# Kernel tuning notes

Measured on AMD Instinct MI355X. Metric: run time of the kernel, lower is better.

Reference implementation:

```python
import jax, jax.numpy as jnp
import numpy as np

BN_EPS = 1e-5
DIST_EPS = 1e-8


def setup_inputs() -> dict:
    key = jax.random.key(0)
    ks = jax.random.split(key, 8)
    B, N, M = 8, 8192, 2048
    C1, C2 = 128, 256
    Cin = C1 + C2  # 384
    H = 256
    return {
        "xyz1": jax.random.normal(ks[0], (B, N, 3), dtype=jnp.float32),
        "xyz2": jax.random.normal(ks[1], (B, M, 3), dtype=jnp.float32),
        "points1": jax.random.normal(ks[2], (B, N, C1), dtype=jnp.float32),
        "points2": jax.random.normal(ks[3], (B, M, C2), dtype=jnp.float32),
        "W1": jax.random.normal(ks[4], (H, Cin), dtype=jnp.float32) * 0.05,
        "b1": jnp.zeros((H,), dtype=jnp.float32),
        "gamma1": jnp.ones((H,), dtype=jnp.float32),
        "beta1": jnp.zeros((H,), dtype=jnp.float32),
        "W2": jax.random.normal(ks[5], (H, H), dtype=jnp.float32) * 0.05,
        "b2": jnp.zeros((H,), dtype=jnp.float32),
        "gamma2": jnp.ones((H,), dtype=jnp.float32),
        "beta2": jnp.zeros((H,), dtype=jnp.float32),
    }


def _interpolate(xyz1, xyz2, points2):
    # squared distances (B,N,M) via the bmm expansion, as in square_distance
    d = (jnp.sum(xyz1 * xyz1, -1)[:, :, None]
         + jnp.sum(xyz2 * xyz2, -1)[:, None, :]
         - 2.0 * jnp.einsum("bnc,bmc->bnm", xyz1, xyz2))
    neg, idx = jax.lax.top_k(-d, 3)          # 3 smallest distances
    dists = -neg                              # (B,N,3)
    recip = 1.0 / (dists + DIST_EPS)
    w = recip / jnp.sum(recip, -1, keepdims=True)  # (B,N,3)
    gathered = jax.vmap(lambda p, i: p[i])(points2, idx)  # (B,N,3,C2)
    return jnp.einsum("bnkc,bnk->bnc", gathered, w)


def _conv_bn_relu(x, W, b, gamma, beta):
    # pointwise conv1d: (B,N,Cin) x (Cout,Cin) -> (B,N,Cout)
    y = jnp.einsum("bnc,oc->bno", x, W) + b
    mean = jnp.mean(y, axis=(0, 1))           # BatchNorm1d (training-mode batch stats)
    var = jnp.var(y, axis=(0, 1))
    y = (y - mean) * jax.lax.rsqrt(var + BN_EPS) * gamma + beta
    return jax.nn.relu(y)


def reference(xyz1, xyz2, points1, points2, W1, b1, gamma1, beta1, W2, b2, gamma2, beta2):
    interp = _interpolate(xyz1, xyz2, points2)          # (B,N,C2)
    x = jnp.concatenate([points1, interp], axis=-1)     # (B,N,C1+C2)
    x = _conv_bn_relu(x, W1, b1, gamma1, beta1)
    x = _conv_bn_relu(x, W2, b2, gamma2, beta2)
    return x  # (B,N,mlp[-1])
```

## Files before the change

kernel.cpp:

```cpp
#include <hip/hip_runtime.h>
#include <hip/hip_bf16.h>
#include <stdint.h>

#define B_SZ  8
#define N_Q   8192
#define M_PT  2048
#define C1    128
#define C2    256
#define CIN   384
#define H_OUT 256
#define R_TOT 65536

#define NCH   8
#define CHM   (M_PT / NCH)
#define QPB   32

typedef __bf16 bf16x8 __attribute__((ext_vector_type(8)));
typedef __bf16 bf16x4 __attribute__((ext_vector_type(4)));
typedef __bf16 bf16x2 __attribute__((ext_vector_type(2)));
typedef float  f32x4  __attribute__((ext_vector_type(4)));

__device__ __forceinline__ void async_copy16(const void* g, void* l) {
    __builtin_amdgcn_global_load_lds(
        (const __attribute__((address_space(1))) unsigned int*)g,
        (__attribute__((address_space(3))) unsigned int*)l,
        16, 0, 0);
}

__global__ __launch_bounds__(256) void f2bf2(const float* __restrict__ a, int na,
                                             const float* __restrict__ b, int nb,
                                             __bf16* __restrict__ oa,
                                             __bf16* __restrict__ ob) {
    int i = blockIdx.x * 256 + threadIdx.x;
    if (i < na)            oa[i] = (__bf16)a[i];
    else if (i - na < nb)  ob[i - na] = (__bf16)b[i - na];
}

__global__ __launch_bounds__(256) void knn_vals(
    const float* __restrict__ xyz1, const float* __restrict__ xyz2,
    float4* __restrict__ vals4) {
    __shared__ float4 pos[CHM];
    const int tid = threadIdx.x;
    const int c   = blockIdx.x & (NCH - 1);
    const int qb  = (blockIdx.x >> 3) & 31;
    const int b   = blockIdx.x >> 8;
    {
        const float* x2 = xyz2 + ((size_t)b * M_PT + c * CHM) * 3;
        float x = x2[tid * 3], y = x2[tid * 3 + 1], z = x2[tid * 3 + 2];
        pos[tid] = make_float4(-2.f * x, -2.f * y, -2.f * z,
                               fmaf(x, x, fmaf(y, y, z * z)));
    }
    __syncthreads();

    const int q = b * N_Q + qb * 256 + tid;
    const float* q1 = xyz1 + (size_t)q * 3;
    float x1 = q1[0], y1 = q1[1], z1 = q1[2];
    float v0 = 3.4e38f, v1 = 3.4e38f, v2 = 3.4e38f;
#pragma unroll 8
    for (int j = 0; j < CHM; ++j) {
        float4 p = pos[j];
        float d  = fmaf(p.x, x1, fmaf(p.y, y1, fmaf(p.z, z1, p.w)));
        float n0 = fminf(d, v0);
        float n1 = __builtin_amdgcn_fmed3f(d, v0, v1);
        float n2 = __builtin_amdgcn_fmed3f(d, v1, v2);
        v0 = n0; v1 = n1; v2 = n2;
    }
    vals4[(size_t)c * R_TOT + q] = make_float4(v0, v1, v2, 0.f);
}

__global__ __launch_bounds__(256) void knn_merge(
    const float4* __restrict__ vals4, const float* __restrict__ xyz1,
    float4* __restrict__ v4, float4* __restrict__ w4) {
    const int q = blockIdx.x * 256 + threadIdx.x;
    float v0 = 3.4e38f, v1 = 3.4e38f, v2 = 3.4e38f;
#pragma unroll
    for (int c = 0; c < NCH; ++c) {
        float4 t = vals4[(size_t)c * R_TOT + q];
#pragma unroll
        for (int k = 0; k < 3; ++k) {
            float d  = (k == 0) ? t.x : (k == 1) ? t.y : t.z;
            float n0 = fminf(d, v0);
            float n1 = __builtin_amdgcn_fmed3f(d, v0, v1);
            float n2 = __builtin_amdgcn_fmed3f(d, v1, v2);
            v0 = n0; v1 = n1; v2 = n2;
        }
    }
    const float* q1 = xyz1 + (size_t)q * 3;
    float x1 = q1[0], y1 = q1[1], z1 = q1[2];
    float n1q = fmaf(x1, x1, fmaf(y1, y1, z1 * z1));
    float r0 = 1.f / ((v0 + n1q) + 1e-8f);
    float r1 = 1.f / ((v1 + n1q) + 1e-8f);
    float r2 = 1.f / ((v2 + n1q) + 1e-8f);
    float rs = 1.f / (r0 + r1 + r2);
    v4[q] = make_float4(v0, v1, v2, 0.f);
    w4[q] = make_float4(r0 * rs, r1 * rs, r2 * rs, 0.f);
}

__global__ __launch_bounds__(256) void knn_recover(
    const float* __restrict__ xyz1, const float* __restrict__ xyz2,
    const float4* __restrict__ v4, int4* __restrict__ ci4) {
    __shared__ float4 pos[CHM];
    const int tid = threadIdx.x;
    const int c   = blockIdx.x & (NCH - 1);
    const int qb  = (blockIdx.x >> 3) & 31;
    const int b   = blockIdx.x >> 8;
    {
        const float* x2 = xyz2 + ((size_t)b * M_PT + c * CHM) * 3;
        float x = x2[tid * 3], y = x2[tid * 3 + 1], z = x2[tid * 3 + 2];
        pos[tid] = make_float4(-2.f * x, -2.f * y, -2.f * z,
                               fmaf(x, x, fmaf(y, y, z * z)));
    }
    __syncthreads();

    const int q = b * N_Q + qb * 256 + tid;
    const float* q1 = xyz1 + (size_t)q * 3;
    float x1 = q1[0], y1 = q1[1], z1 = q1[2];
    const float4 vv = v4[q];
    int i0 = 0x7fffffff, i1 = 0x7fffffff, i2 = 0x7fffffff;
    const int jb = c * CHM;
#pragma unroll 4
    for (int j = 0; j < CHM; ++j) {
        float4 p = pos[j];
        float d  = fmaf(p.x, x1, fmaf(p.y, y1, fmaf(p.z, z1, p.w)));
        if (d <= vv.z) {
            const int jj = jb + j;
            i0 = min(i0, (d == vv.x) ? jj : 0x7fffffff);
            i1 = min(i1, (d == vv.y) ? jj : 0x7fffffff);
            i2 = min(i2, (d == vv.z) ? jj : 0x7fffffff);
        }
    }
    ci4[(size_t)c * R_TOT + q] = make_int4(i0, i1, i2, 0);
}

__global__ __launch_bounds__(256) void interp_gather(
    const float* __restrict__ p1,  const float* __restrict__ p2,
    const int4* __restrict__ ci4,  const float4* __restrict__ w4,
    __bf16* __restrict__ xb) {
    __shared__ float wgt[QPB * 3];
    __shared__ int   ids[QPB * 3];

    const int tid = threadIdx.x;
    const int b   = blockIdx.x >> 8;
    const int q0  = (blockIdx.x & 255) * QPB;

    if (tid < QPB) {
        const int q = b * N_Q + q0 + tid;
        int i0 = 0x7fffffff, i1 = 0x7fffffff, i2 = 0x7fffffff;
#pragma unroll
        for (int c = 0; c < NCH; ++c) {
            int4 t = ci4[(size_t)c * R_TOT + q];
            i0 = min(i0, t.x); i1 = min(i1, t.y); i2 = min(i2, t.z);
        }
        float4 w = w4[q];
        wgt[tid * 3] = w.x; wgt[tid * 3 + 1] = w.y; wgt[tid * 3 + 2] = w.z;
        ids[tid * 3] = i0;  ids[tid * 3 + 1] = i1;  ids[tid * 3 + 2] = i2;
    }
    __syncthreads();

    const int wave = tid >> 6, lane = tid & 63;
    const float* p2b = p2 + (size_t)b * M_PT * C2;
    const float* p1b = p1 + (size_t)(b * N_Q + q0) * C1;
    __bf16* outp = xb + (size_t)(b * N_Q + q0) * CIN;
    for (int qq = wave; qq < QPB; qq += 4) {
        float w0 = wgt[qq * 3], w1 = wgt[qq * 3 + 1], w2 = wgt[qq * 3 + 2];
        int   j0 = ids[qq * 3], j1 = ids[qq * 3 + 1], j2 = ids[qq * 3 + 2];
        const float4* ra = (const float4*)(p2b + (size_t)j0 * C2);
        const float4* rb = (const float4*)(p2b + (size_t)j1 * C2);
        const float4* rc = (const float4*)(p2b + (size_t)j2 * C2);
        float4 va = ra[lane], vb = rb[lane], vc = rc[lane];
        bf16x4 o;
        o[0] = (__bf16)(w0 * va.x + w1 * vb.x + w2 * vc.x);
        o[1] = (__bf16)(w0 * va.y + w1 * vb.y + w2 * vc.y);
        o[2] = (__bf16)(w0 * va.z + w1 * vb.z + w2 * vc.z);
        o[3] = (__bf16)(w0 * va.w + w1 * vb.w + w2 * vc.w);
        *(bf16x4*)(outp + (size_t)qq * CIN + C1 + lane * 4) = o;
        float2 pv = ((const float2*)(p1b + (size_t)qq * C1))[lane];
        bf16x2 o2; o2[0] = (__bf16)pv.x; o2[1] = (__bf16)pv.y;
        *(bf16x2*)(outp + (size_t)qq * CIN + lane * 2) = o2;
    }
}

template <int K, bool OUT_BF16>
__global__ __launch_bounds__(256, 2) void gemm_bt(const __bf16* __restrict__ A,
                                                  const __bf16* __restrict__ Bw,
                                                  void* __restrict__ Cout,
                                                  float* __restrict__ partS,
                                                  float* __restrict__ partQ) {
    __shared__ __attribute__((aligned(16))) __bf16 As[128 * 32];
    __shared__ __attribute__((aligned(16))) __bf16 Bs[128 * 32];
    const int tid  = threadIdx.x;
    const int wave = tid >> 6, lane = tid & 63;
    const int wm = wave >> 1, wn = wave & 1;
    const int quad = lane >> 4, r16 = lane & 15;
    const int bx = blockIdx.x & 1, by = blockIdx.x >> 1;
    const int l4 = lane >> 2, lk = (lane & 3) * 8;

    f32x4 acc[4][4] = {};

    const __bf16* gA = A  + (size_t)(by * 128 + wave * 32 + l4) * K + lk;
    const __bf16* gB = Bw + (size_t)(bx * 128 + wave * 32 + l4) * K + lk;
    char* lA = (char*)As + wave * 2048;
    char* lB = (char*)Bs + wave * 2048;

    for (int k0 = 0; k0 < K; k0 += 32) {
        async_copy16(gA + k0,                  lA);
        async_copy16(gA + k0 + (size_t)16 * K, lA + 1024);
        async_copy16(gB + k0,                  lB);
        async_copy16(gB + k0 + (size_t)16 * K, lB + 1024);
        __syncthreads();

        bf16x8 af[4], bf[4];
#pragma unroll
        for (int t = 0; t < 4; ++t)
            af[t] = *(const bf16x8*)(As + (wm * 64 + t * 16 + r16) * 32 + quad * 8);
#pragma unroll
        for (int u = 0; u < 4; ++u)
            bf[u] = *(const bf16x8*)(Bs + (wn * 64 + u * 16 + r16) * 32 + quad * 8);
#pragma unroll
        for (int t = 0; t < 4; ++t)
#pragma unroll
            for (int u = 0; u < 4; ++u)
                acc[t][u] = __builtin_amdgcn_mfma_f32_16x16x32_bf16(af[t], bf[u], acc[t][u], 0, 0, 0);
        __syncthreads();
    }

#pragma unroll
    for (int t = 0; t < 4; ++t) {
#pragma unroll
        for (int u = 0; u < 4; ++u) {
            const int col = bx * 128 + wn * 64 + u * 16 + r16;
#pragma unroll
            for (int r = 0; r < 4; ++r) {
                const int row = by * 128 + wm * 64 + t * 16 + quad * 4 + r;
                if (OUT_BF16)
                    ((__bf16*)Cout)[(size_t)row * H_OUT + col] = (__bf16)acc[t][u][r];
                else
                    ((float*)Cout)[(size_t)row * H_OUT + col] = acc[t][u][r];
            }
        }
    }

    float* redS = (float*)As;
    float* redQ = ((float*)As) + 1024;
    const int slot = wm * 4 + quad;
#pragma unroll
    for (int u = 0; u < 4; ++u) {
        float s = 0.f, qq = 0.f;
#pragma unroll
        for (int t = 0; t < 4; ++t)
#pragma unroll
            for (int r = 0; r < 4; ++r) { float v = acc[t][u][r]; s += v; qq = fmaf(v, v, qq); }
        const int col = wn * 64 + u * 16 + r16;
        redS[col * 8 + slot] = s;
        redQ[col * 8 + slot] = qq;
    }
    __syncthreads();
    if (tid < 128) {
        float s = 0.f, qq = 0.f;
#pragma unroll
        for (int k = 0; k < 8; ++k) { s += redS[tid * 8 + k]; qq += redQ[tid * 8 + k]; }
        partS[(size_t)blockIdx.x * 128 + tid] = s;
        partQ[(size_t)blockIdx.x * 128 + tid] = qq;
    }
}

__global__ __launch_bounds__(256) void bn_finalize(const float* __restrict__ pS,
                                                   const float* __restrict__ pQ,
                                                   const float* __restrict__ gamma,
                                                   const float* __restrict__ beta,
                                                   float* __restrict__ sc,
                                                   float* __restrict__ sh) {
    __shared__ float rs[256], rq[256];
    const int c = blockIdx.x;
    const int t = threadIdx.x;
    const int half = c >> 7, lo = c & 127;
    const size_t o1 = (size_t)(2 * t + half) * 128 + lo;
    const size_t o2 = (size_t)(2 * (t + 256) + half) * 128 + lo;
    rs[t] = pS[o1] + pS[o2];
    rq[t] = pQ[o1] + pQ[o2];
    __syncthreads();
    for (int k = 128; k > 0; k >>= 1) {
        if (t < k) { rs[t] += rs[t + k]; rq[t] += rq[t + k]; }
        __syncthreads();
    }
    if (t == 0) {
        const float inv = 1.f / (float)R_TOT;
        float mean = rs[0] * inv;
        float var  = rq[0] * inv - mean * mean;
        float a    = gamma[c] * rsqrtf(var + 1e-5f);
        sc[c] = a;
        sh[c] = beta[c] - mean * a;
    }
}

__global__ __launch_bounds__(256) void apply_bf16(__bf16* __restrict__ y,
                                                  const float* __restrict__ sc,
                                                  const float* __restrict__ sh) {
    __shared__ float scs[256], shs[256];
    scs[threadIdx.x] = sc[threadIdx.x];
    shs[threadIdx.x] = sh[threadIdx.x];
    __syncthreads();
    size_t i = ((size_t)blockIdx.x * 256 + threadIdx.x) * 8;
    int c0 = (int)(i & 255);
    bf16x8 v = *(const bf16x8*)(y + i);
#pragma unroll
    for (int e = 0; e < 8; ++e) {
        float f = fmaf((float)v[e], scs[c0 + e], shs[c0 + e]);
        v[e] = (__bf16)fmaxf(f, 0.f);
    }
    *(bf16x8*)(y + i) = v;
}

__global__ __launch_bounds__(256) void apply_f32(float* __restrict__ y,
                                                 const float* __restrict__ sc,
                                                 const float* __restrict__ sh) {
    __shared__ float scs[256], shs[256];
    scs[threadIdx.x] = sc[threadIdx.x];
    shs[threadIdx.x] = sh[threadIdx.x];
    __syncthreads();
    size_t i = ((size_t)blockIdx.x * 256 + threadIdx.x) * 4;
    int c0 = (int)(i & 255);
    float4 v = *(const float4*)(y + i);
    v.x = fmaxf(fmaf(v.x, scs[c0 + 0], shs[c0 + 0]), 0.f);
    v.y = fmaxf(fmaf(v.y, scs[c0 + 1], shs[c0 + 1]), 0.f);
    v.z = fmaxf(fmaf(v.z, scs[c0 + 2], shs[c0 + 2]), 0.f);
    v.w = fmaxf(fmaf(v.w, scs[c0 + 3], shs[c0 + 3]), 0.f);
    *(float4*)(y + i) = v;
}

extern "C" void kernel_launch(void* const* d_in, const int* in_sizes, int n_in,
                              void* d_out, int out_size, void* d_ws, size_t ws_size,
                              hipStream_t stream) {
    const float* xyz1 = (const float*)d_in[0];
    const float* xyz2 = (const float*)d_in[1];
    const float* p1   = (const float*)d_in[2];
    const float* p2   = (const float*)d_in[3];
    const float* W1   = (const float*)d_in[4];
    const float* g1   = (const float*)d_in[6];
    const float* be1  = (const float*)d_in[7];
    const float* W2   = (const float*)d_in[8];
    const float* g2   = (const float*)d_in[10];
    const float* be2  = (const float*)d_in[11];
    float* out = (float*)d_out;

    char* ws = (char*)d_ws;
    __bf16* xb     = (__bf16*)(ws);
    __bf16* y1b    = (__bf16*)(ws + 50331648);
    float4* vals4  = (float4*)(ws + 50331648);
    int4*   ci4    = (int4*)  (ws + 58720256);
    float4* v4     = (float4*)(ws + 67108864);
    float4* w4     = (float4*)(ws + 68157440);
    __bf16* wb1    = (__bf16*)(ws + 83886080);
    __bf16* wb2    = (__bf16*)(ws + 84082688);
    float*  sc1    = (float*) (ws + 84213760);
    float*  sh1    = sc1 + 256;
    float*  sc2    = sc1 + 512;
    float*  sh2    = sc1 + 768;

    float* partS1 = (float*)d_out;
    float* partQ1 = partS1 + 131072;
    float* partS2 = (float*)ws;
    float* partQ2 = partS2 + 131072;

    f2bf2<<<640, 256, 0, stream>>>(W1, H_OUT * CIN, W2, H_OUT * H_OUT, wb1, wb2);

    knn_vals<<<B_SZ * 32 * NCH, 256, 0, stream>>>(xyz1, xyz2, vals4);
    knn_merge<<<R_TOT / 256, 256, 0, stream>>>(vals4, xyz1, v4, w4);
    knn_recover<<<B_SZ * 32 * NCH, 256, 0, stream>>>(xyz1, xyz2, v4, ci4);
    interp_gather<<<R_TOT / QPB, 256, 0, stream>>>(p1, p2, ci4, w4, xb);

    gemm_bt<CIN, true><<<1024, 256, 0, stream>>>(xb, wb1, (void*)y1b, partS1, partQ1);
    bn_finalize<<<256, 256, 0, stream>>>(partS1, partQ1, g1, be1, sc1, sh1);
    apply_bf16<<<8192, 256, 0, stream>>>(y1b, sc1, sh1);

    gemm_bt<H_OUT, false><<<1024, 256, 0, stream>>>(y1b, wb2, (void*)out, partS2, partQ2);
    bn_finalize<<<256, 256, 0, stream>>>(partS2, partQ2, g2, be2, sc2, sh2);
    apply_f32<<<16384, 256, 0, stream>>>(out, sc2, sh2);
}
```

Baseline: 280.4 us.

## Fuse KNN stages into one kernel and store second GEMM output as bf16

The chunked KNN pipeline (vals, merge, recover) and the weight conversion kernel are merged into a single kernel in which each block scans all 2048 points from LDS. That block computes the weights and recovers the indices directly, so the partial-result buffers and the merge pass disappear. The second GEMM now writes bf16 to workspace, and the final BN/ReLU kernel reads bf16 and writes fp32 output, halving the intermediate traffic. The cost is that the KNN grid shrinks from 2048 to 256 blocks, which risks under-occupying the GPU on the compute-bound distance scan, and the extra bf16 rounding of the final pre-BN values may reduce accuracy.

```diff
diff --git a/kernel.cpp b/kernel.cpp
--- a/kernel.cpp
+++ b/kernel.cpp
@@ -11,8 +11,6 @@
 #define H_OUT 256
 #define R_TOT 65536
 
-#define NCH   8
-#define CHM   (M_PT / NCH)
 #define QPB   32
 
 typedef __bf16 bf16x8 __attribute__((ext_vector_type(8)));
@@ -27,37 +25,38 @@
         16, 0, 0);
 }
 
-__global__ __launch_bounds__(256) void f2bf2(const float* __restrict__ a, int na,
-                                             const float* __restrict__ b, int nb,
-                                             __bf16* __restrict__ oa,
-                                             __bf16* __restrict__ ob) {
-    int i = blockIdx.x * 256 + threadIdx.x;
-    if (i < na)            oa[i] = (__bf16)a[i];
-    else if (i - na < nb)  ob[i - na] = (__bf16)b[i - na];
-}
-
-__global__ __launch_bounds__(256) void knn_vals(
+__global__ __launch_bounds__(256) void knn_fused(
     const float* __restrict__ xyz1, const float* __restrict__ xyz2,
-    float4* __restrict__ vals4) {
-    __shared__ float4 pos[CHM];
+    const float* __restrict__ W1,   const float* __restrict__ W2,
+    __bf16* __restrict__ wb1,       __bf16* __restrict__ wb2,
+    float4* __restrict__ w4,        int4* __restrict__ ci4) {
+    __shared__ float4 pos[M_PT];
     const int tid = threadIdx.x;
-    const int c   = blockIdx.x & (NCH - 1);
-    const int qb  = (blockIdx.x >> 3) & 31;
-    const int b   = blockIdx.x >> 8;
+    const int b   = blockIdx.x >> 5;
+    const int qb  = blockIdx.x & 31;
+
     {
-        const float* x2 = xyz2 + ((size_t)b * M_PT + c * CHM) * 3;
-        float x = x2[tid * 3], y = x2[tid * 3 + 1], z = x2[tid * 3 + 2];
-        pos[tid] = make_float4(-2.f * x, -2.f * y, -2.f * z,
-                               fmaf(x, x, fmaf(y, y, z * z)));
+        const int g = blockIdx.x * 256 + tid;
+        wb1[g] = (__bf16)W1[g];
+        if (g < H_OUT * CIN - R_TOT) wb1[R_TOT + g] = (__bf16)W1[R_TOT + g];
+        wb2[g] = (__bf16)W2[g];
+    }
+
+    const float* x2 = xyz2 + (size_t)b * M_PT * 3;
+    for (int j = tid; j < M_PT; j += 256) {
+        float x = x2[j * 3], y = x2[j * 3 + 1], z = x2[j * 3 + 2];
+        pos[j] = make_float4(-2.f * x, -2.f * y, -2.f * z,
+                             fmaf(x, x, fmaf(y, y, z * z)));
     }
     __syncthreads();
 
     const int q = b * N_Q + qb * 256 + tid;
     const float* q1 = xyz1 + (size_t)q * 3;
-    float x1 = q1[0], y1 = q1[1], z1 = q1[2];
+    const float x1 = q1[0], y1 = q1[1], z1 = q1[2];
+
     float v0 = 3.4e38f, v1 = 3.4e38f, v2 = 3.4e38f;
 #pragma unroll 8
-    for (int j = 0; j < CHM; ++j) {
+    for (int j = 0; j < M_PT; ++j) {
         float4 p = pos[j];
         float d  = fmaf(p.x, x1, fmaf(p.y, y1, fmaf(p.z, z1, p.w)));
         float n0 = fminf(d, v0);
@@ -65,71 +64,28 @@
         float n2 = __builtin_amdgcn_fmed3f(d, v1, v2);
         v0 = n0; v1 = n1; v2 = n2;
     }
-    vals4[(size_t)c * R_TOT + q] = make_float4(v0, v1, v2, 0.f);
-}
-
-__global__ __launch_bounds__(256) void knn_merge(
-    const float4* __restrict__ vals4, const float* __restrict__ xyz1,
-    float4* __restrict__ v4, float4* __restrict__ w4) {
-    const int q = blockIdx.x * 256 + threadIdx.x;
-    float v0 = 3.4e38f, v1 = 3.4e38f, v2 = 3.4e38f;
-#pragma unroll
-    for (int c = 0; c < NCH; ++c) {
-        float4 t = vals4[(size_t)c * R_TOT + q];
-#pragma unroll
-        for (int k = 0; k < 3; ++k) {
-            float d  = (k == 0) ? t.x : (k == 1) ? t.y : t.z;
-            float n0 = fminf(d, v0);
-            float n1 = __builtin_amdgcn_fmed3f(d, v0, v1);
-            float n2 = __builtin_amdgcn_fmed3f(d, v1, v2);
-            v0 = n0; v1 = n1; v2 = n2;
-        }
-    }
-    const float* q1 = xyz1 + (size_t)q * 3;
-    float x1 = q1[0], y1 = q1[1], z1 = q1[2];
-    float n1q = fmaf(x1, x1, fmaf(y1, y1, z1 * z1));
-    float r0 = 1.f / ((v0 + n1q) + 1e-8f);
-    float r1 = 1.f / ((v1 + n1q) + 1e-8f);
-    float r2 = 1.f / ((v2 + n1q) + 1e-8f);
-    float rs = 1.f / (r0 + r1 + r2);
-    v4[q] = make_float4(v0, v1, v2, 0.f);
-    w4[q] = make_float4(r0 * rs, r1 * rs, r2 * rs, 0.f);
-}
-
-__global__ __launch_bounds__(256) void knn_recover(
-    const float* __restrict__ xyz1, const float* __restrict__ xyz2,
-    const float4* __restrict__ v4, int4* __restrict__ ci4) {
-    __shared__ float4 pos[CHM];
-    const int tid = threadIdx.x;
-    const int c   = blockIdx.x & (NCH - 1);
-    const int qb  = (blockIdx.x >> 3) & 31;
-    const int b   = blockIdx.x >> 8;
+
     {
-        const float* x2 = xyz2 + ((size_t)b * M_PT + c * CHM) * 3;
-        float x = x2[tid * 3], y = x2[tid * 3 + 1], z = x2[tid * 3 + 2];
-        pos[tid] = make_float4(-2.f * x, -2.f * y, -2.f * z,
-                               fmaf(x, x, fmaf(y, y, z * z)));
-    }
-    __syncthreads();
-
-    const int q = b * N_Q + qb * 256 + tid;
-    const float* q1 = xyz1 + (size_t)q * 3;
-    float x1 = q1[0], y1 = q1[1], z1 = q1[2];
-    const float4 vv = v4[q];
+        float n1q = fmaf(x1, x1, fmaf(y1, y1, z1 * z1));
+        float r0 = 1.f / ((v0 + n1q) + 1e-8f);
+        float r1 = 1.f / ((v1 + n1q) + 1e-8f);
+        float r2 = 1.f / ((v2 + n1q) + 1e-8f);
+        float rs = 1.f / (r0 + r1 + r2);
+        w4[q] = make_float4(r0 * rs, r1 * rs, r2 * rs, 0.f);
+    }
+
     int i0 = 0x7fffffff, i1 = 0x7fffffff, i2 = 0x7fffffff;
-    const int jb = c * CHM;
 #pragma unroll 4
-    for (int j = 0; j < CHM; ++j) {
+    for (int j = 0; j < M_PT; ++j) {
         float4 p = pos[j];
         float d  = fmaf(p.x, x1, fmaf(p.y, y1, fmaf(p.z, z1, p.w)));
-        if (d <= vv.z) {
-            const int jj = jb + j;
-            i0 = min(i0, (d == vv.x) ? jj : 0x7fffffff);
-            i1 = min(i1, (d == vv.y) ? jj : 0x7fffffff);
-            i2 = min(i2, (d == vv.z) ? jj : 0x7fffffff);
+        if (d <= v2) {
+            i0 = min(i0, (d == v0) ? j : 0x7fffffff);
+            i1 = min(i1, (d == v1) ? j : 0x7fffffff);
+            i2 = min(i2, (d == v2) ? j : 0x7fffffff);
         }
     }
-    ci4[(size_t)c * R_TOT + q] = make_int4(i0, i1, i2, 0);
+    ci4[q] = make_int4(i0, i1, i2, 0);
 }
 
 __global__ __launch_bounds__(256) void interp_gather(
@@ -145,15 +101,10 @@
 
     if (tid < QPB) {
         const int q = b * N_Q + q0 + tid;
-        int i0 = 0x7fffffff, i1 = 0x7fffffff, i2 = 0x7fffffff;
-#pragma unroll
-        for (int c = 0; c < NCH; ++c) {
-            int4 t = ci4[(size_t)c * R_TOT + q];
-            i0 = min(i0, t.x); i1 = min(i1, t.y); i2 = min(i2, t.z);
-        }
-        float4 w = w4[q];
-        wgt[tid * 3] = w.x; wgt[tid * 3 + 1] = w.y; wgt[tid * 3 + 2] = w.z;
-        ids[tid * 3] = i0;  ids[tid * 3 + 1] = i1;  ids[tid * 3 + 2] = i2;
+        int4   ii = ci4[q];
+        float4 w  = w4[q];
+        wgt[tid * 3] = w.x;  wgt[tid * 3 + 1] = w.y;  wgt[tid * 3 + 2] = w.z;
+        ids[tid * 3] = ii.x; ids[tid * 3 + 1] = ii.y; ids[tid * 3 + 2] = ii.z;
     }
     __syncthreads();
 
@@ -180,10 +131,10 @@
     }
 }
 
-template <int K, bool OUT_BF16>
+template <int K>
 __global__ __launch_bounds__(256, 2) void gemm_bt(const __bf16* __restrict__ A,
                                                   const __bf16* __restrict__ Bw,
-                                                  void* __restrict__ Cout,
+                                                  __bf16* __restrict__ Cout,
                                                   float* __restrict__ partS,
                                                   float* __restrict__ partQ) {
     __shared__ __attribute__((aligned(16))) __bf16 As[128 * 32];
@@ -232,10 +183,7 @@
 #pragma unroll
             for (int r = 0; r < 4; ++r) {
                 const int row = by * 128 + wm * 64 + t * 16 + quad * 4 + r;
-                if (OUT_BF16)
-                    ((__bf16*)Cout)[(size_t)row * H_OUT + col] = (__bf16)acc[t][u][r];
-                else
-                    ((float*)Cout)[(size_t)row * H_OUT + col] = acc[t][u][r];
+                Cout[(size_t)row * H_OUT + col] = (__bf16)acc[t][u][r];
             }
         }
     }
@@ -311,21 +259,26 @@
     *(bf16x8*)(y + i) = v;
 }
 
-__global__ __launch_bounds__(256) void apply_f32(float* __restrict__ y,
+__global__ __launch_bounds__(256) void apply_out(const __bf16* __restrict__ y,
                                                  const float* __restrict__ sc,
-                                                 const float* __restrict__ sh) {
+                                                 const float* __restrict__ sh,
+                                                 float* __restrict__ out) {
     __shared__ float scs[256], shs[256];
     scs[threadIdx.x] = sc[threadIdx.x];
     shs[threadIdx.x] = sh[threadIdx.x];
     __syncthreads();
-    size_t i = ((size_t)blockIdx.x * 256 + threadIdx.x) * 4;
+    size_t i = ((size_t)blockIdx.x * 256 + threadIdx.x) * 8;
     int c0 = (int)(i & 255);
-    float4 v = *(const float4*)(y + i);
-    v.x = fmaxf(fmaf(v.x, scs[c0 + 0], shs[c0 + 0]), 0.f);
-    v.y = fmaxf(fmaf(v.y, scs[c0 + 1], shs[c0 + 1]), 0.f);
-    v.z = fmaxf(fmaf(v.z, scs[c0 + 2], shs[c0 + 2]), 0.f);
-    v.w = fmaxf(fmaf(v.w, scs[c0 + 3], shs[c0 + 3]), 0.f);
-    *(float4*)(y + i) = v;
+    bf16x8 v = *(const bf16x8*)(y + i);
+    f32x4 o0, o1;
+#pragma unroll
+    for (int e = 0; e < 4; ++e)
+        o0[e] = fmaxf(fmaf((float)v[e], scs[c0 + e], shs[c0 + e]), 0.f);
+#pragma unroll
+    for (int e = 0; e < 4; ++e)
+        o1[e] = fmaxf(fmaf((float)v[4 + e], scs[c0 + 4 + e], shs[c0 + 4 + e]), 0.f);
+    *(f32x4*)(out + i)     = o0;
+    *(f32x4*)(out + i + 4) = o1;
 }
 
 extern "C" void kernel_launch(void* const* d_in, const int* in_sizes, int n_in,
@@ -346,10 +299,11 @@
     char* ws = (char*)d_ws;
     __bf16* xb     = (__bf16*)(ws);
     __bf16* y1b    = (__bf16*)(ws + 50331648);
-    float4* vals4  = (float4*)(ws + 50331648);
-    int4*   ci4    = (int4*)  (ws + 58720256);
-    float4* v4     = (float4*)(ws + 67108864);
-    float4* w4     = (float4*)(ws + 68157440);
+    float4* w4     = (float4*)(ws + 50331648);
+    int4*   ci4    = (int4*)  (ws + 51380224);
+    __bf16* y2b    = (__bf16*)(ws);
+    float*  partS2 = (float*) (ws + 35651584);
+    float*  partQ2 = partS2 + 131072;
     __bf16* wb1    = (__bf16*)(ws + 83886080);
     __bf16* wb2    = (__bf16*)(ws + 84082688);
     float*  sc1    = (float*) (ws + 84213760);
@@ -359,21 +313,15 @@
 
     float* partS1 = (float*)d_out;
     float* partQ1 = partS1 + 131072;
-    float* partS2 = (float*)ws;
-    float* partQ2 = partS2 + 131072;
-
-    f2bf2<<<640, 256, 0, stream>>>(W1, H_OUT * CIN, W2, H_OUT * H_OUT, wb1, wb2);
-
-    knn_vals<<<B_SZ * 32 * NCH, 256, 0, stream>>>(xyz1, xyz2, vals4);
-    knn_merge<<<R_TOT / 256, 256, 0, stream>>>(vals4, xyz1, v4, w4);
-    knn_recover<<<B_SZ * 32 * NCH, 256, 0, stream>>>(xyz1, xyz2, v4, ci4);
+
+    knn_fused<<<256, 256, 0, stream>>>(xyz1, xyz2, W1, W2, wb1, wb2, w4, ci4);
     interp_gather<<<R_TOT / QPB, 256, 0, stream>>>(p1, p2, ci4, w4, xb);
 
-    gemm_bt<CIN, true><<<1024, 256, 0, stream>>>(xb, wb1, (void*)y1b, partS1, partQ1);
+    gemm_bt<CIN><<<1024, 256, 0, stream>>>(xb, wb1, y1b, partS1, partQ1);
     bn_finalize<<<256, 256, 0, stream>>>(partS1, partQ1, g1, be1, sc1, sh1);
     apply_bf16<<<8192, 256, 0, stream>>>(y1b, sc1, sh1);
 
-    gemm_bt<H_OUT, false><<<1024, 256, 0, stream>>>(y1b, wb2, (void*)out, partS2, partQ2);
+    gemm_bt<H_OUT><<<1024, 256, 0, stream>>>(y1b, wb2, y2b, partS2, partQ2);
     bn_finalize<<<256, 256, 0, stream>>>(partS2, partQ2, g2, be2, sc2, sh2);
-    apply_f32<<<16384, 256, 0, stream>>>(out, sc2, sh2);
-}
+    apply_out<<<8192, 256, 0, stream>>>(y2b, sc2, sh2, out);
+}
```

Result: slower. 398.6 us (+42.1%).
